# Kernel optimization log

Measured on AMD Instinct MI355X. Metric: run time of the kernel, lower is better.

The kernel has to match this reference:

```python
import jax, jax.numpy as jnp
import numpy as np

B, T, D_IN, D_HID, D_OUT = 64, 4096, 128, 128, 128
LN_EPS = 1e-5


def setup_inputs() -> dict:
    key = jax.random.key(0)
    ks = jax.random.split(key, 10)
    s_in = 1.0 / np.sqrt(D_IN)
    s_cat = 1.0 / np.sqrt(D_IN + D_HID)
    return {
        "x": jax.random.normal(ks[0], (B, T, D_IN), dtype=jnp.float32),
        "graph": jax.random.uniform(ks[1], (D_HID, D_HID), dtype=jnp.float32),
        # message_transform: Linear(D_IN -> D_HID), stored as (in, out)
        "W_msg": jax.random.uniform(ks[2], (D_IN, D_HID), jnp.float32, -s_in, s_in),
        "b_msg": jax.random.uniform(ks[3], (D_HID,), jnp.float32, -s_in, s_in),
        # update_fn[0]: Linear(D_IN + D_HID -> D_IN)
        "W_upd": jax.random.uniform(ks[4], (D_IN + D_HID, D_IN), jnp.float32, -s_cat, s_cat),
        "b_upd": jax.random.uniform(ks[5], (D_IN,), jnp.float32, -s_cat, s_cat),
        # output_proj: Linear(D_IN -> D_OUT)
        "W_out": jax.random.uniform(ks[6], (D_IN, D_OUT), jnp.float32, -s_in, s_in),
        "b_out": jax.random.uniform(ks[7], (D_OUT,), jnp.float32, -s_in, s_in),
        # LayerNorm(D_OUT)
        "gamma": jnp.ones((D_OUT,), dtype=jnp.float32),
        "beta": jnp.zeros((D_OUT,), dtype=jnp.float32),
    }


def reference(x, graph, W_msg, b_msg, W_upd, b_upd, W_out, b_out, gamma, beta):
    # message: shared linear transform over features -> [B, T, D_HID]
    msg = jnp.einsum("bti,ih->bth", x, W_msg) + b_msg
    # aggregate ('sum'): latent adjacency over the feature axis -> [B, T, D_HID]
    agg = jnp.einsum("bth,hg->btg", msg, graph)
    # update: concat -> Linear -> exact GELU (Dropout is identity in eval)
    combined = jnp.concatenate([x, agg], axis=-1)  # [B, T, D_IN + D_HID]
    h = jax.nn.gelu(jnp.einsum("btc,co->bto", combined, W_upd) + b_upd,
                    approximate=False)
    # output projection + LayerNorm over last dim
    out = jnp.einsum("bti,io->bto", h, W_out) + b_out
    mu = jnp.mean(out, axis=-1, keepdims=True)
    var = jnp.var(out, axis=-1, keepdims=True)
    return (out - mu) * jax.lax.rsqrt(var + LN_EPS) * gamma + beta
```

## Files before the change

kernel.cpp:

```cpp
#include <hip/hip_runtime.h>
#include <math.h>


#define D 128
#define NROWS (64 * 4096)

typedef __bf16 bf16x8 __attribute__((ext_vector_type(8)));
typedef float  f32x4  __attribute__((ext_vector_type(4)));

__device__ __forceinline__ int wswz(int o, int i) {
    return o * 128 + ((((i >> 3) ^ (o & 15)) & 15) << 3) + (i & 7);
}

__global__ __launch_bounds__(256) void prep1(
    const float* __restrict__ W_msg, const float* __restrict__ graph,
    const float* __restrict__ b_msg, const float* __restrict__ W_out,
    float* __restrict__ G2, float* __restrict__ b2tmp, __bf16* __restrict__ W2s) {
    __shared__ float gs[D * D];
    const int tid = threadIdx.x;
    {
        const float4* g4 = (const float4*)graph;
        float4* s4 = (float4*)gs;
#pragma unroll
        for (int it = 0; it < (D * D / 4) / 256; ++it)
            s4[tid + it * 256] = g4[tid + it * 256];
    }
    __syncthreads();
    const int i0 = blockIdx.x * 8;
#pragma unroll
    for (int p = 0; p < 4; ++p) {
        const int flat = tid + p * 256;
        const int i = i0 + (flat >> 7);
        const int g = flat & 127;
        const float* wrow = W_msg + i * D;
        float s = 0.f;
#pragma unroll 8
        for (int h = 0; h < D; ++h) s += wrow[h] * gs[h * D + g];
        G2[i * D + g] = s;
        W2s[wswz(g, i)] = (__bf16)W_out[i * D + g];
    }
    if (blockIdx.x == 0 && tid < 128) {
        float sb = 0.f;
#pragma unroll 8
        for (int h = 0; h < D; ++h) sb += b_msg[h] * gs[h * D + tid];
        b2tmp[tid] = sb;
    }
}

__global__ __launch_bounds__(256) void prep2(
    const float* __restrict__ W_upd, const float* __restrict__ b_upd,
    const float* __restrict__ G2, const float* __restrict__ b2tmp,
    __bf16* __restrict__ W1s, float* __restrict__ b_eff) {
    __shared__ float wls[D * D];
    const int tid = threadIdx.x;
    {
        const float4* w4 = (const float4*)(W_upd + D * D);
        float4* s4 = (float4*)wls;
#pragma unroll
        for (int it = 0; it < (D * D / 4) / 256; ++it)
            s4[tid + it * 256] = w4[tid + it * 256];
    }
    __syncthreads();
    const int i0 = blockIdx.x * 8;
#pragma unroll
    for (int p = 0; p < 4; ++p) {
        const int flat = tid + p * 256;
        const int i = i0 + (flat >> 7);
        const int o = flat & 127;
        const float* g2row = G2 + i * D;
        float s = W_upd[i * D + o];
#pragma unroll 8
        for (int g = 0; g < D; ++g) s += g2row[g] * wls[g * D + o];
        W1s[wswz(o, i)] = (__bf16)s;
    }
    if (blockIdx.x == 0 && tid < 128) {
        float sb = b_upd[tid];
#pragma unroll 8
        for (int g = 0; g < D; ++g) sb += b2tmp[g] * wls[g * D + tid];
        b_eff[tid] = sb;
    }
}

__device__ __forceinline__ float gelu_fast(float v) {
    const float u = 1.5957691216057308f * v * (1.0f + 0.044715f * v * v);
    return v / (1.0f + __expf(-u));
}

__global__ __launch_bounds__(256) void fused_main(
    const float* __restrict__ x, const __bf16* __restrict__ Wsrc,
    const float* __restrict__ b1, const float* __restrict__ b2,
    const float* __restrict__ gamma, const float* __restrict__ beta,
    float* __restrict__ out) {

    __shared__ __align__(16) __bf16 Wlds[2 * 128 * 128];
    __shared__ __align__(16) __bf16 tf[4][16 * 128];

    const int tid = threadIdx.x;
    {
        const float4* src4 = (const float4*)Wsrc;
        float4* dst4 = (float4*)Wlds;
#pragma unroll
        for (int it = 0; it < 16; ++it) dst4[it * 256 + tid] = src4[it * 256 + tid];
    }

    const int w = tid >> 6;
    const int l = tid & 63;
    const int q = l >> 4;
    const int m = l & 15;
    __bf16* tfw = &tf[w][0];

    float b1v[8], b2v[8], gv[8], bv[8];
#pragma unroll
    for (int t = 0; t < 8; ++t) {
        const int c = t * 16 + m;
        b1v[t] = b1[c]; b2v[t] = b2[c]; gv[t] = gamma[c]; bv[t] = beta[c];
    }

    __syncthreads();

    const int rowbase0 = blockIdx.x * 256 + w * 64;

    float4 xr[8];
    {
        const float* xrow = x + (size_t)(rowbase0 + m) * D;
#pragma unroll
        for (int ks = 0; ks < 4; ++ks) {
            const float4* xp = (const float4*)(xrow + ks * 32 + q * 8);
            xr[2 * ks]     = xp[0];
            xr[2 * ks + 1] = xp[1];
        }
    }

    for (int tile = 0; tile < 4; ++tile) {
        const int rowbase = rowbase0 + tile * 16;

        float4 xn[8];
        if (tile < 3) {
            const float* xnrow = x + (size_t)(rowbase + 16 + m) * D;
#pragma unroll
            for (int ks = 0; ks < 4; ++ks) {
                const float4* xp = (const float4*)(xnrow + ks * 32 + q * 8);
                xn[2 * ks]     = xp[0];
                xn[2 * ks + 1] = xp[1];
            }
        }

        bf16x8 a[4];
#pragma unroll
        for (int ks = 0; ks < 4; ++ks) {
            const float4 xa = xr[2 * ks], xb = xr[2 * ks + 1];
            a[ks][0] = (__bf16)xa.x; a[ks][1] = (__bf16)xa.y;
            a[ks][2] = (__bf16)xa.z; a[ks][3] = (__bf16)xa.w;
            a[ks][4] = (__bf16)xb.x; a[ks][5] = (__bf16)xb.y;
            a[ks][6] = (__bf16)xb.z; a[ks][7] = (__bf16)xb.w;
        }

        f32x4 acc[8];
#pragma unroll
        for (int t = 0; t < 8; ++t) acc[t] = (f32x4)(0.0f);
#pragma unroll
        for (int ks = 0; ks < 4; ++ks) {
            const int blk = (((ks * 4 + q) ^ m) & 15) << 3;
#pragma unroll
            for (int t = 0; t < 8; ++t) {
                const bf16x8 bfr = *(const bf16x8*)&Wlds[(t * 16 + m) * 128 + blk];
                acc[t] = __builtin_amdgcn_mfma_f32_16x16x32_bf16(a[ks], bfr, acc[t], 0, 0, 0);
            }
        }

#pragma unroll
        for (int t = 0; t < 8; ++t) {
#pragma unroll
            for (int j = 0; j < 4; ++j) {
                const float v = acc[t][j] + b1v[t];
                const int r = q * 4 + j;
                const int blk = (((t * 2 + (m >> 3)) ^ r) & 15) << 3;
                tfw[r * 128 + blk + (m & 7)] = (__bf16)gelu_fast(v);
            }
        }
        __syncthreads();

        f32x4 acc2[8];
#pragma unroll
        for (int t = 0; t < 8; ++t) acc2[t] = (f32x4)(0.0f);
#pragma unroll
        for (int ks = 0; ks < 4; ++ks) {
            const int blk = (((ks * 4 + q) ^ m) & 15) << 3;
            const bf16x8 af = *(const bf16x8*)&tfw[m * 128 + blk];
#pragma unroll
            for (int t = 0; t < 8; ++t) {
                const bf16x8 bfr = *(const bf16x8*)&Wlds[16384 + (t * 16 + m) * 128 + blk];
                acc2[t] = __builtin_amdgcn_mfma_f32_16x16x32_bf16(af, bfr, acc2[t], 0, 0, 0);
            }
        }
        __syncthreads();

        float vsum[4] = {0.f, 0.f, 0.f, 0.f}, vsq[4] = {0.f, 0.f, 0.f, 0.f};
#pragma unroll
        for (int t = 0; t < 8; ++t) {
#pragma unroll
            for (int j = 0; j < 4; ++j) {
                const float v = acc2[t][j] + b2v[t];
                acc2[t][j] = v;
                vsum[j] += v;
                vsq[j] += v * v;
            }
        }
#pragma unroll
        for (int j = 0; j < 4; ++j) {
#pragma unroll
            for (int mask = 1; mask <= 8; mask <<= 1) {
                vsum[j] += __shfl_xor(vsum[j], mask);
                vsq[j]  += __shfl_xor(vsq[j], mask);
            }
        }
#pragma unroll
        for (int j = 0; j < 4; ++j) {
            const float mu = vsum[j] * (1.0f / 128.0f);
            const float var = vsq[j] * (1.0f / 128.0f) - mu * mu;
            const float rstd = rsqrtf(var + 1e-5f);
            float* orow = out + (size_t)(rowbase + q * 4 + j) * D;
#pragma unroll
            for (int t = 0; t < 8; ++t)
                orow[t * 16 + m] = (acc2[t][j] - mu) * rstd * gv[t] + bv[t];
        }

        if (tile < 3) {
#pragma unroll
            for (int k = 0; k < 8; ++k) xr[k] = xn[k];
        }
    }
}

extern "C" void kernel_launch(void* const* d_in, const int* in_sizes, int n_in,
                              void* d_out, int out_size, void* d_ws, size_t ws_size,
                              hipStream_t stream) {
    const float* x     = (const float*)d_in[0];
    const float* graph = (const float*)d_in[1];
    const float* W_msg = (const float*)d_in[2];
    const float* b_msg = (const float*)d_in[3];
    const float* W_upd = (const float*)d_in[4];
    const float* b_upd = (const float*)d_in[5];
    const float* W_out = (const float*)d_in[6];
    const float* b_out = (const float*)d_in[7];
    const float* gamma = (const float*)d_in[8];
    const float* beta  = (const float*)d_in[9];
    float* out = (float*)d_out;

    char* ws = (char*)d_ws;
    __bf16* W1s   = (__bf16*)(ws + 0);
    __bf16* W2s   = (__bf16*)(ws + 32768);
    float*  G2    = (float*)(ws + 65536);
    float*  b2tmp = (float*)(ws + 131072);
    float*  b_eff = (float*)(ws + 131584);

    prep1<<<16, 256, 0, stream>>>(W_msg, graph, b_msg, W_out, G2, b2tmp, W2s);
    prep2<<<16, 256, 0, stream>>>(W_upd, b_upd, G2, b2tmp, W1s, b_eff);
    fused_main<<<NROWS / 256, 256, 0, stream>>>(x, W1s, b_eff, b_out, gamma, beta, out);
}
```

Before: 293.8 us.

## Keep GELU intermediate in registers via transposed MFMA and ds_bpermute

The first GEMM now uses swapped MFMA operands, so each lane holds outputs along the feature axis. The GELU results are packed to bf16 and redistributed into A-fragments with ds_bpermute, which removes the LDS staging buffer and both __syncthreads per tile. Each lane now writes float4 outputs, LayerNorm reduction needs only two shuffles, and the bias, gamma and beta vectors sit in LDS. Blocks grow to 512 threads, which halves the number of per-block weight loads into LDS, at some cost in register pressure.

Result: slower. 692.2 us (+135.6%).

```diff
diff --git a/kernel.cpp b/kernel.cpp
--- a/kernel.cpp
+++ b/kernel.cpp
@@ -6,7 +6,9 @@
 #define NROWS (64 * 4096)
 
 typedef __bf16 bf16x8 __attribute__((ext_vector_type(8)));
+typedef __bf16 bf16x2 __attribute__((ext_vector_type(2)));
 typedef float  f32x4  __attribute__((ext_vector_type(4)));
+typedef int    i32x4  __attribute__((ext_vector_type(4)));
 
 __device__ __forceinline__ int wswz(int o, int i) {
     return o * 128 + ((((i >> 3) ^ (o & 15)) & 15) << 3) + (i & 7);
@@ -86,48 +88,63 @@
     return v / (1.0f + __expf(-u));
 }
 
-__global__ __launch_bounds__(256) void fused_main(
+__device__ __forceinline__ uint32_t pkbf16(float x, float y) {
+    bf16x2 p;
+    p[0] = (__bf16)x;
+    p[1] = (__bf16)y;
+    return __builtin_bit_cast(uint32_t, p);
+}
+
+__global__ __launch_bounds__(512, 4) void fused_main(
     const float* __restrict__ x, const __bf16* __restrict__ Wsrc,
     const float* __restrict__ b1, const float* __restrict__ b2,
     const float* __restrict__ gamma, const float* __restrict__ beta,
     float* __restrict__ out) {
 
     __shared__ __align__(16) __bf16 Wlds[2 * 128 * 128];
-    __shared__ __align__(16) __bf16 tf[4][16 * 128];
+    __shared__ __align__(16) float b1s[128];
+    __shared__ __align__(16) float b2s[128];
+    __shared__ __align__(16) float gms[128];
+    __shared__ __align__(16) float bts[128];
 
     const int tid = threadIdx.x;
     {
         const float4* src4 = (const float4*)Wsrc;
         float4* dst4 = (float4*)Wlds;
 #pragma unroll
-        for (int it = 0; it < 16; ++it) dst4[it * 256 + tid] = src4[it * 256 + tid];
+        for (int it = 0; it < 8; ++it) dst4[it * 512 + tid] = src4[it * 512 + tid];
+    }
+    if (tid < 128) {
+        b1s[tid] = b1[tid];
+        b2s[tid] = b2[tid];
+        gms[tid] = gamma[tid];
+        bts[tid] = beta[tid];
     }
 
     const int w = tid >> 6;
     const int l = tid & 63;
     const int q = l >> 4;
     const int m = l & 15;
-    __bf16* tfw = &tf[w][0];
-
-    float b1v[8], b2v[8], gv[8], bv[8];
-#pragma unroll
-    for (int t = 0; t < 8; ++t) {
-        const int c = t * 16 + m;
-        b1v[t] = b1[c]; b2v[t] = b2[c]; gv[t] = gamma[c]; bv[t] = beta[c];
-    }
+
+    const int addrA = ((((2 * q) & 3) << 4) | m) << 2;
+    const int addrB = addrA + 64;
+    const bool qhi = (q & 2) != 0;
 
     __syncthreads();
 
-    const int rowbase0 = blockIdx.x * 256 + w * 64;
-
-    float4 xr[8];
+    const int rowbase0 = blockIdx.x * 512 + w * 64;
+
+    bf16x8 a[4];
     {
         const float* xrow = x + (size_t)(rowbase0 + m) * D;
 #pragma unroll
         for (int ks = 0; ks < 4; ++ks) {
             const float4* xp = (const float4*)(xrow + ks * 32 + q * 8);
-            xr[2 * ks]     = xp[0];
-            xr[2 * ks + 1] = xp[1];
+            const float4 xa = xp[0], xb = xp[1];
+            a[ks][0] = (__bf16)xa.x; a[ks][1] = (__bf16)xa.y;
+            a[ks][2] = (__bf16)xa.z; a[ks][3] = (__bf16)xa.w;
+            a[ks][4] = (__bf16)xb.x; a[ks][5] = (__bf16)xb.y;
+            a[ks][6] = (__bf16)xb.z; a[ks][7] = (__bf16)xb.w;
         }
     }
 
@@ -145,16 +162,6 @@
             }
         }
 
-        bf16x8 a[4];
-#pragma unroll
-        for (int ks = 0; ks < 4; ++ks) {
-            const float4 xa = xr[2 * ks], xb = xr[2 * ks + 1];
-            a[ks][0] = (__bf16)xa.x; a[ks][1] = (__bf16)xa.y;
-            a[ks][2] = (__bf16)xa.z; a[ks][3] = (__bf16)xa.w;
-            a[ks][4] = (__bf16)xb.x; a[ks][5] = (__bf16)xb.y;
-            a[ks][6] = (__bf16)xb.z; a[ks][7] = (__bf16)xb.w;
-        }
-
         f32x4 acc[8];
 #pragma unroll
         for (int t = 0; t < 8; ++t) acc[t] = (f32x4)(0.0f);
@@ -163,71 +170,97 @@
             const int blk = (((ks * 4 + q) ^ m) & 15) << 3;
 #pragma unroll
             for (int t = 0; t < 8; ++t) {
-                const bf16x8 bfr = *(const bf16x8*)&Wlds[(t * 16 + m) * 128 + blk];
-                acc[t] = __builtin_amdgcn_mfma_f32_16x16x32_bf16(a[ks], bfr, acc[t], 0, 0, 0);
-            }
-        }
-
+                const bf16x8 wf = *(const bf16x8*)&Wlds[(t * 16 + m) * 128 + blk];
+                acc[t] = __builtin_amdgcn_mfma_f32_16x16x32_bf16(wf, a[ks], acc[t], 0, 0, 0);
+            }
+        }
+
+        uint32_t lov[8], hiv[8];
 #pragma unroll
         for (int t = 0; t < 8; ++t) {
+            const f32x4 bq = *(const f32x4*)&b1s[t * 16 + q * 4];
+            lov[t] = pkbf16(gelu_fast(acc[t][0] + bq[0]), gelu_fast(acc[t][1] + bq[1]));
+            hiv[t] = pkbf16(gelu_fast(acc[t][2] + bq[2]), gelu_fast(acc[t][3] + bq[3]));
+        }
+
+        bf16x8 hf[4];
+#pragma unroll
+        for (int ks = 0; ks < 4; ++ks) {
+            const int l0 = (int)lov[2 * ks], l1 = (int)lov[2 * ks + 1];
+            const int h0 = (int)hiv[2 * ks], h1 = (int)hiv[2 * ks + 1];
+            const int w0a = __builtin_amdgcn_ds_bpermute(addrA, l0);
+            const int w0b = __builtin_amdgcn_ds_bpermute(addrA, l1);
+            const int w1a = __builtin_amdgcn_ds_bpermute(addrA, h0);
+            const int w1b = __builtin_amdgcn_ds_bpermute(addrA, h1);
+            const int w2a = __builtin_amdgcn_ds_bpermute(addrB, l0);
+            const int w2b = __builtin_amdgcn_ds_bpermute(addrB, l1);
+            const int w3a = __builtin_amdgcn_ds_bpermute(addrB, h0);
+            const int w3b = __builtin_amdgcn_ds_bpermute(addrB, h1);
+            i32x4 wv;
+            wv[0] = qhi ? w0b : w0a;
+            wv[1] = qhi ? w1b : w1a;
+            wv[2] = qhi ? w2b : w2a;
+            wv[3] = qhi ? w3b : w3a;
+            hf[ks] = __builtin_bit_cast(bf16x8, wv);
+        }
+
+        if (tile < 3) {
+#pragma unroll
+            for (int ks = 0; ks < 4; ++ks) {
+                const float4 xa = xn[2 * ks], xb = xn[2 * ks + 1];
+                a[ks][0] = (__bf16)xa.x; a[ks][1] = (__bf16)xa.y;
+                a[ks][2] = (__bf16)xa.z; a[ks][3] = (__bf16)xa.w;
+                a[ks][4] = (__bf16)xb.x; a[ks][5] = (__bf16)xb.y;
+                a[ks][6] = (__bf16)xb.z; a[ks][7] = (__bf16)xb.w;
+            }
+        }
+
+        f32x4 acc2[8];
+#pragma unroll
+        for (int t = 0; t < 8; ++t) acc2[t] = (f32x4)(0.0f);
+#pragma unroll
+        for (int ks = 0; ks < 4; ++ks) {
+            const int blk = (((ks * 4 + q) ^ m) & 15) << 3;
+#pragma unroll
+            for (int t = 0; t < 8; ++t) {
+                const bf16x8 wf = *(const bf16x8*)&Wlds[16384 + (t * 16 + m) * 128 + blk];
+                acc2[t] = __builtin_amdgcn_mfma_f32_16x16x32_bf16(wf, hf[ks], acc2[t], 0, 0, 0);
+            }
+        }
+
+        float vs = 0.f, vq = 0.f;
+#pragma unroll
+        for (int t = 0; t < 8; ++t) {
+            const f32x4 bq = *(const f32x4*)&b2s[t * 16 + q * 4];
 #pragma unroll
             for (int j = 0; j < 4; ++j) {
-                const float v = acc[t][j] + b1v[t];
-                const int r = q * 4 + j;
-                const int blk = (((t * 2 + (m >> 3)) ^ r) & 15) << 3;
-                tfw[r * 128 + blk + (m & 7)] = (__bf16)gelu_fast(v);
-            }
-        }
-        __syncthreads();
-
-        f32x4 acc2[8];
-#pragma unroll
-        for (int t = 0; t < 8; ++t) acc2[t] = (f32x4)(0.0f);
-#pragma unroll
-        for (int ks = 0; ks < 4; ++ks) {
-            const int blk = (((ks * 4 + q) ^ m) & 15) << 3;
-            const bf16x8 af = *(const bf16x8*)&tfw[m * 128 + blk];
-#pragma unroll
-            for (int t = 0; t < 8; ++t) {
-                const bf16x8 bfr = *(const bf16x8*)&Wlds[16384 + (t * 16 + m) * 128 + blk];
-                acc2[t] = __builtin_amdgcn_mfma_f32_16x16x32_bf16(af, bfr, acc2[t], 0, 0, 0);
-            }
-        }
-        __syncthreads();
-
-        float vsum[4] = {0.f, 0.f, 0.f, 0.f}, vsq[4] = {0.f, 0.f, 0.f, 0.f};
+                const float v = acc2[t][j] + bq[j];
+                acc2[t][j] = v;
+                vs += v;
+                vq += v * v;
+            }
+        }
+        vs += __shfl_xor(vs, 16);
+        vq += __shfl_xor(vq, 16);
+        vs += __shfl_xor(vs, 32);
+        vq += __shfl_xor(vq, 32);
+
+        const float mu = vs * (1.0f / 128.0f);
+        const float var = vq * (1.0f / 128.0f) - mu * mu;
+        const float rstd = rsqrtf(var + 1e-5f);
+        const float nmr = -mu * rstd;
+
+        float* orow = out + (size_t)(rowbase + m) * D;
 #pragma unroll
         for (int t = 0; t < 8; ++t) {
-#pragma unroll
-            for (int j = 0; j < 4; ++j) {
-                const float v = acc2[t][j] + b2v[t];
-                acc2[t][j] = v;
-                vsum[j] += v;
-                vsq[j] += v * v;
-            }
-        }
-#pragma unroll
-        for (int j = 0; j < 4; ++j) {
-#pragma unroll
-            for (int mask = 1; mask <= 8; mask <<= 1) {
-                vsum[j] += __shfl_xor(vsum[j], mask);
-                vsq[j]  += __shfl_xor(vsq[j], mask);
-            }
-        }
-#pragma unroll
-        for (int j = 0; j < 4; ++j) {
-            const float mu = vsum[j] * (1.0f / 128.0f);
-            const float var = vsq[j] * (1.0f / 128.0f) - mu * mu;
-            const float rstd = rsqrtf(var + 1e-5f);
-            float* orow = out + (size_t)(rowbase + q * 4 + j) * D;
-#pragma unroll
-            for (int t = 0; t < 8; ++t)
-                orow[t * 16 + m] = (acc2[t][j] - mu) * rstd * gv[t] + bv[t];
-        }
-
-        if (tile < 3) {
-#pragma unroll
-            for (int k = 0; k < 8; ++k) xr[k] = xn[k];
+            const f32x4 gq = *(const f32x4*)&gms[t * 16 + q * 4];
+            const f32x4 bq = *(const f32x4*)&bts[t * 16 + q * 4];
+            float4 res;
+            res.x = fmaf(fmaf(acc2[t][0], rstd, nmr), gq[0], bq[0]);
+            res.y = fmaf(fmaf(acc2[t][1], rstd, nmr), gq[1], bq[1]);
+            res.z = fmaf(fmaf(acc2[t][2], rstd, nmr), gq[2], bq[2]);
+            res.w = fmaf(fmaf(acc2[t][3], rstd, nmr), gq[3], bq[3]);
+            *(float4*)(orow + t * 16 + q * 4) = res;
         }
     }
 }
@@ -256,5 +289,5 @@
 
     prep1<<<16, 256, 0, stream>>>(W_msg, graph, b_msg, W_out, G2, b2tmp, W2s);
     prep2<<<16, 256, 0, stream>>>(W_upd, b_upd, G2, b2tmp, W1s, b_eff);
-    fused_main<<<NROWS / 256, 256, 0, stream>>>(x, W1s, b_eff, b_out, gamma, beta, out);
-}
+    fused_main<<<NROWS / 512, 512, 0, stream>>>(x, W1s, b_eff, b_out, gamma, beta, out);
+}
```
